# Performance work log

Hardware: AMD Instinct MI355X
Metric: run time of the kernel (lower is better)

Reference implementation:

```python
import jax, jax.numpy as jnp
import numpy as np

VOCAB = 10000
EMBED = 100
T = 80
UNITS = 512
B = 4096
RATE = 0.2  # Keras LSTMCell dropout on inputs, 4 gate masks, cached across timesteps


def setup_inputs() -> dict:
    key = jax.random.key(0)
    ks = jax.random.split(key, 10)
    s = 0.05
    return {
        "inputs": jax.random.randint(ks[0], (B, T), 0, VOCAB, dtype=jnp.int32),
        "embed": jax.random.normal(ks[1], (VOCAB, EMBED), dtype=jnp.float32) * s,
        "W0": jax.random.normal(ks[2], (EMBED, 4 * UNITS), dtype=jnp.float32) * s,
        "U0": jax.random.normal(ks[3], (UNITS, 4 * UNITS), dtype=jnp.float32) * s,
        "b0": jnp.zeros((4 * UNITS,), dtype=jnp.float32),
        "W1": jax.random.normal(ks[4], (UNITS, 4 * UNITS), dtype=jnp.float32) * s,
        "U1": jax.random.normal(ks[5], (UNITS, 4 * UNITS), dtype=jnp.float32) * s,
        "b1": jnp.zeros((4 * UNITS,), dtype=jnp.float32),
        "Wout": jax.random.normal(ks[6], (UNITS, 1), dtype=jnp.float32) * s,
        "bout": jnp.zeros((1,), dtype=jnp.float32),
    }


def _dropout_masks(key, shape):
    keep = 1.0 - RATE
    return jax.random.bernoulli(key, keep, shape).astype(jnp.float32) / keep


def _lstm_cell(h, c, xt, masks, W, U, b, in_dim):
    # masks: [4, B, in_dim] per-gate input dropout masks (fixed across time)
    # kernel layout: W.reshape(in_dim, 4, UNITS), gate order i, f, g(cand), o
    z = jnp.einsum('gbd,dgh->bgh', xt[None] * masks, W.reshape(in_dim, 4, UNITS))
    z = z + (h @ U + b).reshape(-1, 4, UNITS)
    i = jax.nn.sigmoid(z[:, 0])
    f = jax.nn.sigmoid(z[:, 1])
    g = jnp.tanh(z[:, 2])
    o = jax.nn.sigmoid(z[:, 3])
    c_new = f * c + i * g
    h_new = o * jnp.tanh(c_new)
    return h_new, c_new


def reference(inputs, embed, W0, U0, b0, W1, U1, b1, Wout, bout):
    x = embed[inputs]                      # [B, T, EMBED]
    mkey = jax.random.key(42)
    k0, k1 = jax.random.split(mkey)
    m0 = _dropout_masks(k0, (4, B, EMBED))
    m1 = _dropout_masks(k1, (4, B, UNITS))

    def step(carry, xt):
        h0, c0, h1, c1 = carry
        h0, c0 = _lstm_cell(h0, c0, xt, m0, W0, U0, b0, EMBED)
        h1, c1 = _lstm_cell(h1, c1, h0, m1, W1, U1, b1, UNITS)
        return (h0, c0, h1, c1), None

    init = tuple(jnp.zeros((B, UNITS), dtype=jnp.float32) for _ in range(4))
    (h0, c0, h1, c1), _ = jax.lax.scan(step, init, jnp.swapaxes(x, 0, 1))
    return jax.nn.sigmoid(h1 @ Wout + bout)   # [B, 1]
```

## Files before the change

### kernel.cpp

```cpp
#include <hip/hip_runtime.h>
#include <hip/hip_bf16.h>
#include <stdint.h>

#define BATCH 4096
#define TT    80
#define EMB   100
#define UNITS 512
#define K0P   128

typedef unsigned short ushort;
typedef unsigned char uchar;
typedef __bf16 bf16x8 __attribute__((ext_vector_type(8)));
typedef float f32x4 __attribute__((ext_vector_type(4)));
typedef uint32_t u32x4 __attribute__((ext_vector_type(4)));

__device__ __forceinline__ uint32_t rotl32(uint32_t x, uint32_t r) {
  return (x << r) | (x >> (32u - r));
}
__device__ __forceinline__ void tf_round4(uint32_t& x0, uint32_t& x1,
                                          int r0, int r1, int r2, int r3) {
  x0 += x1; x1 = rotl32(x1, r0); x1 ^= x0;
  x0 += x1; x1 = rotl32(x1, r1); x1 ^= x0;
  x0 += x1; x1 = rotl32(x1, r2); x1 ^= x0;
  x0 += x1; x1 = rotl32(x1, r3); x1 ^= x0;
}
__device__ __forceinline__ void tf2x32(uint32_t k0, uint32_t k1,
                                       uint32_t x0, uint32_t x1,
                                       uint32_t& y0, uint32_t& y1) {
  uint32_t k2 = k0 ^ k1 ^ 0x1BD11BDAu;
  x0 += k0; x1 += k1;
  tf_round4(x0, x1, 13, 15, 26, 6);  x0 += k1; x1 += k2 + 1u;
  tf_round4(x0, x1, 17, 29, 16, 24); x0 += k2; x1 += k0 + 2u;
  tf_round4(x0, x1, 13, 15, 26, 6);  x0 += k0; x1 += k1 + 3u;
  tf_round4(x0, x1, 17, 29, 16, 24); x0 += k1; x1 += k2 + 4u;
  tf_round4(x0, x1, 13, 15, 26, 6);  x0 += k2; x1 += k0 + 5u;
  y0 = x0; y1 = x1;
}
__device__ __forceinline__ int keepbit(uint32_t u) {
  float f = __uint_as_float((u >> 9) | 0x3F800000u) - 1.0f;
  return f < 0.8f ? 1 : 0;
}
__device__ __forceinline__ ushort f2bf(float f) {
  uint32_t u = __float_as_uint(f);
  uint32_t r = (u + 0x7FFFu + ((u >> 16) & 1u)) >> 16;
  return (ushort)r;
}
__device__ __forceinline__ float bf2f(ushort u) {
  return __uint_as_float(((uint32_t)u) << 16);
}

__global__ __launch_bounds__(256) void masksB(uchar* __restrict__ m0B,
                                              uchar* __restrict__ m1B) {
  uint32_t k0a, k0b, k1a, k1b;
  tf2x32(0u, 42u, 0u, 0u, k0a, k0b);
  tf2x32(0u, 42u, 0u, 1u, k1a, k1b);
  const int T0 = 4 * BATCH * K0P;
  const int T1 = 4 * BATCH * UNITS;
  for (int i = blockIdx.x * blockDim.x + threadIdx.x; i < T0 + T1;
       i += gridDim.x * blockDim.x) {
    if (i < T0) {
      const int g = i >> 19, b = (i >> 7) & 4095, k = i & 127;
      uchar v = 0;
      if (k < EMB) {
        uint32_t y0, y1;
        tf2x32(k0a, k0b, 0u, (uint32_t)(g * (BATCH * EMB) + b * EMB + k), y0, y1);
        v = keepbit(y0 ^ y1) ? 0xFFu : 0u;
      }
      m0B[i] = v;
    } else {
      const int j = i - T0;
      const int g = j >> 21, b = (j >> 9) & 4095, k = j & 511;
      uint32_t y0, y1;
      tf2x32(k1a, k1b, 0u, (uint32_t)(g * (BATCH * UNITS) + b * UNITS + k), y0, y1);
      m1B[j] = keepbit(y0 ^ y1) ? 0xFFu : 0u;
    }
  }
}

__global__ __launch_bounds__(256) void convT(const float* __restrict__ src,
                                             ushort* __restrict__ dst,
                                             int Ksrc, int Kpad, float scale) {
  __shared__ float t[32][33];
  const int n0 = blockIdx.x * 32, kk0 = blockIdx.y * 32;
  const int tx = threadIdx.x & 31, ty = threadIdx.x >> 5;
#pragma unroll
  for (int r = ty; r < 32; r += 8) {
    const int k = kk0 + r;
    t[r][tx] = (k < Ksrc) ? src[(size_t)k * 2048 + n0 + tx] : 0.f;
  }
  __syncthreads();
#pragma unroll
  for (int r = ty; r < 32; r += 8)
    dst[(size_t)(n0 + r) * Kpad + kk0 + tx] = f2bf(scale * t[tx][r]);
}

__global__ __launch_bounds__(256) void xprep3(const int* __restrict__ inputs,
                                              const float* __restrict__ embed,
                                              ushort* __restrict__ X0,
                                              ushort* __restrict__ X1,
                                              ushort* __restrict__ X2) {
  const int i = blockIdx.x * 256 + threadIdx.x;
  const int s = i >> 16, r = i & 65535;
  const int b = r >> 4, k = (r & 15) * 8;
  ushort* X = (s == 0) ? X0 : (s == 1) ? X1 : X2;
  const int idx = inputs[b * TT + s];
  ushort v[8];
#pragma unroll
  for (int j = 0; j < 8; j++) {
    const int kk = k + j;
    v[j] = (kk < EMB) ? f2bf(embed[(size_t)idx * EMB + kk]) : (ushort)0;
  }
  *(bf16x8*)(X + (size_t)b * K0P + k) = *(bf16x8*)v;
}

__device__ __forceinline__ void gload16(const void* g, void* l) {
  __builtin_amdgcn_global_load_lds(
      (const __attribute__((address_space(1))) unsigned int*)g,
      (__attribute__((address_space(3))) unsigned int*)l, 16, 0, 0);
}

template <bool MASKED>
__device__ __forceinline__ void gemm_seg(
    const ushort* __restrict__ A, int K, const ushort* __restrict__ Bw,
    const uchar* __restrict__ mB, int bm0, int bh0, int tid,
    ushort* As, ushort* Bs, f32x4 acc[4][8]) {
  const int w = tid >> 6, l = tid & 63;
  const int wr = w >> 1, wc = w & 1;
  const int fr = l & 15, kq = l >> 4;
  const int srow = l >> 2, schunk = (l & 3) * 8;

#pragma unroll 1
  for (int k0 = 0; k0 < K; k0 += 32) {
#pragma unroll
    for (int c2 = 0; c2 < 2; c2++) {
      const int rt = w + c2 * 4;
      gload16(A + (size_t)(bm0 + rt * 16 + srow) * K + k0 + schunk,
              As + rt * 512);
    }
#pragma unroll
    for (int c2 = 0; c2 < 4; c2++) {
      const int ct = w * 4 + c2;
      const int col = ct * 16 + srow;
      const int nrow = (col >> 6) * 512 + bh0 + (col & 63);
      gload16(Bw + (size_t)nrow * K + k0 + schunk, Bs + ct * 512);
    }
    uint2 md[4][4];
    if (MASKED) {
#pragma unroll
      for (int fi = 0; fi < 4; fi++) {
        const int row = bm0 + wr * 64 + fi * 16 + fr;
#pragma unroll
        for (int g = 0; g < 4; g++)
          md[fi][g] = *(const uint2*)(mB + (size_t)(g * BATCH + row) * K + k0 +
                                      kq * 8);
      }
    }
    __syncthreads();

    u32x4 af[4];
    bf16x8 bf[8];
#pragma unroll
    for (int fi = 0; fi < 4; fi++)
      af[fi] = *(const u32x4*)&As[(wr * 64 + fi * 16 + fr) * 32 + kq * 8];
#pragma unroll
    for (int g = 0; g < 4; g++)
#pragma unroll
      for (int hf = 0; hf < 2; hf++)
        bf[g * 2 + hf] =
            *(const bf16x8*)&Bs[((g * 4 + wc * 2 + hf) * 16 + fr) * 32 + kq * 8];

#pragma unroll
    for (int g = 0; g < 4; g++) {
#pragma unroll
      for (int fi = 0; fi < 4; fi++) {
        u32x4 ua = af[fi];
        if (MASKED) {
          const uint2 m = md[fi][g];
          ua.x &= __builtin_amdgcn_perm(m.x, m.x, 0x01010000u);
          ua.y &= __builtin_amdgcn_perm(m.x, m.x, 0x03030202u);
          ua.z &= __builtin_amdgcn_perm(m.y, m.y, 0x01010000u);
          ua.w &= __builtin_amdgcn_perm(m.y, m.y, 0x03030202u);
        }
        const bf16x8 a = __builtin_bit_cast(bf16x8, ua);
        acc[fi][g * 2 + 0] = __builtin_amdgcn_mfma_f32_16x16x32_bf16(
            a, bf[g * 2 + 0], acc[fi][g * 2 + 0], 0, 0, 0);
        acc[fi][g * 2 + 1] = __builtin_amdgcn_mfma_f32_16x16x32_bf16(
            a, bf[g * 2 + 1], acc[fi][g * 2 + 1], 0, 0, 0);
      }
    }
    __syncthreads();
  }
}

__global__ __launch_bounds__(256, 2) void fused_step(
    int nl1,
    const ushort* __restrict__ h0b_cur, const ushort* __restrict__ h1b_prev,
    ushort* __restrict__ h1b_out, float* __restrict__ c1f,
    const ushort* __restrict__ W1T, const ushort* __restrict__ U1T,
    const float* __restrict__ b1, int nl0, const ushort* __restrict__ Xcur,
    ushort* __restrict__ h0b_out, float* __restrict__ c0f,
    const ushort* __restrict__ W0T, const ushort* __restrict__ U0T,
    const float* __restrict__ b0, const uchar* __restrict__ mask1B,
    const uchar* __restrict__ mask0B, int tprep, const int* __restrict__ inputs,
    const float* __restrict__ embed, ushort* __restrict__ Xprep) {
  __shared__ __align__(16) ushort smem[12288];
  const int bid = blockIdx.x, tid = threadIdx.x;
  const bool isl1 = bid < nl1;
  const int lbid = isl1 ? bid : bid - nl1;
  const int cid = (lbid & 7) * 32 + (lbid >> 3);
  const int bm0 = (cid >> 3) * 128;
  const int bh0 = (cid & 7) * 64;
  const int w = tid >> 6, l = tid & 63;
  const int wr = w >> 1, wc = w & 1;
  const int fr = l & 15, kq = l >> 4;

  const ushort *Amask, *Aun, *BW, *BU;
  const float* bias;
  const uchar* mB;
  float* cblob;
  ushort* hout;
  int Km;
  if (isl1) {
    Amask = h0b_cur; Km = UNITS; Aun = h1b_prev; BW = W1T; BU = U1T;
    bias = b1; mB = mask1B; cblob = c1f; hout = h1b_out;
  } else {
    Amask = Xcur; Km = K0P; Aun = h0b_cur; BW = W0T; BU = U0T;
    bias = b0; mB = mask0B; cblob = c0f; hout = h0b_out;
  }

  f32x4 acc[4][8] = {};
  ushort* As = smem;
  ushort* Bs = smem + 4096;

  gemm_seg<true>(Amask, Km, BW, mB, bm0, bh0, tid, As, Bs, acc);
  gemm_seg<false>(Aun, UNITS, BU, nullptr, bm0, bh0, tid, As, Bs, acc);

  float* cb = cblob + (size_t)cid * 8192 + tid * 32;
  f32x4 cold[8];
#pragma unroll
  for (int q = 0; q < 8; q++) cold[q] = *(const f32x4*)(cb + q * 4);

  float bi[2], bfv[2], bg[2], bo[2];
#pragma unroll
  for (int hf = 0; hf < 2; hf++) {
    const int h = bh0 + wc * 32 + hf * 16 + fr;
    bi[hf] = bias[h];
    bfv[hf] = bias[512 + h];
    bg[hf] = bias[1024 + h];
    bo[hf] = bias[1536 + h];
  }

  f32x4 cnew[8];
#pragma unroll
  for (int fi = 0; fi < 4; fi++) {
#pragma unroll
    for (int hf = 0; hf < 2; hf++) {
#pragma unroll
      for (int jj = 0; jj < 4; jj++) {
        const float zi = acc[fi][0 + hf][jj] + bi[hf];
        const float zf = acc[fi][2 + hf][jj] + bfv[hf];
        const float zg = acc[fi][4 + hf][jj] + bg[hf];
        const float zo = acc[fi][6 + hf][jj] + bo[hf];
        const float iv = 1.f / (1.f + __expf(-zi));
        const float fv = 1.f / (1.f + __expf(-zf));
        const float gv = tanhf(zg);
        const float ov = 1.f / (1.f + __expf(-zo));
        const float cn = fv * cold[fi * 2 + hf][jj] + iv * gv;
        cnew[fi * 2 + hf][jj] = cn;
        const float hn = ov * tanhf(cn);
        const int rloc = wr * 64 + fi * 16 + kq * 4 + jj;
        const int hloc = wc * 32 + hf * 16 + fr;
        smem[rloc * 64 + hloc] = f2bf(hn);
      }
    }
  }
#pragma unroll
  for (int q = 0; q < 8; q++) *(f32x4*)(cb + q * 4) = cnew[q];
  __syncthreads();

#pragma unroll
  for (int c2 = 0; c2 < 4; c2++) {
    const int idx = c2 * 256 + tid;
    const int rloc = idx >> 3, hcol = (idx & 7) * 8;
    *(bf16x8*)(hout + (size_t)(bm0 + rloc) * UNITS + bh0 + hcol) =
        *(const bf16x8*)&smem[rloc * 64 + hcol];
  }

  if (!isl1 && tprep >= 0) {
    const int base = lbid * 2048 + tid * 8;
    const int b = base >> 7, k = base & 127;
    const int idx = inputs[b * TT + tprep];
    ushort v[8];
#pragma unroll
    for (int j = 0; j < 8; j++) {
      const int kk = k + j;
      v[j] = (kk < EMB) ? f2bf(embed[(size_t)idx * EMB + kk]) : (ushort)0;
    }
    *(bf16x8*)(Xprep + (size_t)b * K0P + k) = *(bf16x8*)v;
  }
}

__global__ __launch_bounds__(256) void out_kernel(const ushort* __restrict__ h1b,
                                                  const float* __restrict__ Wout,
                                                  const float* __restrict__ bout,
                                                  float* __restrict__ out) {
  const int wid = (blockIdx.x * blockDim.x + threadIdx.x) >> 6;
  const int lane = threadIdx.x & 63;
  if (wid >= BATCH) return;
  const ushort* hr = h1b + (size_t)wid * UNITS;
  float s = 0.f;
#pragma unroll
  for (int j = 0; j < UNITS; j += 64) s += bf2f(hr[j + lane]) * Wout[j + lane];
  for (int off = 32; off; off >>= 1) s += __shfl_down(s, off, 64);
  if (lane == 0) out[wid] = 1.f / (1.f + __expf(-(s + bout[0])));
}

extern "C" void kernel_launch(void* const* d_in, const int* in_sizes, int n_in,
                              void* d_out, int out_size, void* d_ws, size_t ws_size,
                              hipStream_t stream) {
  const int* inputs = (const int*)d_in[0];
  const float* embed = (const float*)d_in[1];
  const float* W0 = (const float*)d_in[2];
  const float* U0 = (const float*)d_in[3];
  const float* b0 = (const float*)d_in[4];
  const float* W1 = (const float*)d_in[5];
  const float* U1 = (const float*)d_in[6];
  const float* b1 = (const float*)d_in[7];
  const float* Wout = (const float*)d_in[8];
  const float* bout = (const float*)d_in[9];
  float* out = (float*)d_out;

  char* ws = (char*)d_ws;
  const size_t MB = 1 << 20;
  float* c0f    = (float*)(ws);
  float* c1f    = (float*)(ws + 8 * MB);
  ushort* h0b1  = (ushort*)(ws + 16 * MB);
  ushort* h1b1  = (ushort*)(ws + 20 * MB);
  ushort* h0b0  = (ushort*)(ws + 24 * MB);
  ushort* h1b0  = (ushort*)(ws + 28 * MB);
  ushort* X0    = (ushort*)(ws + 32 * MB);
  ushort* X1    = (ushort*)(ws + 33 * MB);
  ushort* X2    = (ushort*)(ws + 34 * MB);
  ushort* W0T   = (ushort*)(ws + 35 * MB);
  ushort* U0T   = (ushort*)(ws + 36 * MB);
  ushort* W1T   = (ushort*)(ws + 38 * MB);
  ushort* U1T   = (ushort*)(ws + 40 * MB);
  uchar* m0B    = (uchar*)(ws + 42 * MB);
  uchar* m1B    = (uchar*)(ws + 44 * MB);

  ushort* h0b[2] = {h0b0, h0b1};
  ushort* h1b[2] = {h1b0, h1b1};
  ushort* X[3] = {X0, X1, X2};

  hipMemsetAsync(ws, 0, 24 * MB, stream);

  masksB<<<8192, 256, 0, stream>>>(m0B, m1B);
  {
    dim3 g0(2048 / 32, K0P / 32);
    convT<<<g0, 256, 0, stream>>>(W0, W0T, EMB, K0P, 1.25f);
    dim3 g1(2048 / 32, UNITS / 32);
    convT<<<g1, 256, 0, stream>>>(U0, U0T, UNITS, UNITS, 1.0f);
    convT<<<g1, 256, 0, stream>>>(W1, W1T, UNITS, UNITS, 1.25f);
    convT<<<g1, 256, 0, stream>>>(U1, U1T, UNITS, UNITS, 1.0f);
  }
  xprep3<<<768, 256, 0, stream>>>(inputs, embed, X0, X1, X2);

  fused_step<<<256, 256, 0, stream>>>(
      0, h0b[1], h1b[1], h1b[0], c1f, W1T, U1T, b1,
      256, X[0], h0b[0], c0f, W0T, U0T, b0, m1B, m0B,
      -1, inputs, embed, X[0]);

  for (int k = 0; k < TT; k++) {
    const int p = k & 1;
    const int nl0 = (k < TT - 1) ? 256 : 0;
    const int tprep = (k + 3 < TT) ? (k + 3) : -1;
    fused_step<<<256 + nl0, 256, 0, stream>>>(
        256, h0b[p], h1b[p ^ 1], h1b[p], c1f, W1T, U1T, b1,
        nl0, X[(k + 1) % 3], h0b[p ^ 1], c0f, W0T, U0T, b0, m1B, m0B,
        tprep, inputs, embed, X[k % 3]);
  }

  out_kernel<<<BATCH * 64 / 256, 256, 0, stream>>>(h1b[1], Wout, bout, out);
}
```

Before: 6.276 ms.

## Replace per-timestep launches with a persistent kernel using a global atomic barrier

The 81 per-step fused_step launches become one persistent kernel of 512 blocks. Blocks loop over the phases and sync through a spin-wait atomic grid barrier. The cell state now stays in registers across steps instead of round-tripping through global memory, and embedding prefetch moves to a double buffer. The mask loads move inside the MFMA loop to cut register pressure. This removes launch overhead and c-state traffic, but relies on all 512 blocks being co-resident (2 per CU) and adds barrier latency.

```diff
diff --git a/kernel.cpp b/kernel.cpp
--- a/kernel.cpp
+++ b/kernel.cpp
@@ -7,6 +7,7 @@
 #define EMB   100
 #define UNITS 512
 #define K0P   128
+#define NBLK  512
 
 typedef unsigned short ushort;
 typedef unsigned char uchar;
@@ -94,21 +95,22 @@
     dst[(size_t)(n0 + r) * Kpad + kk0 + tx] = f2bf(scale * t[tx][r]);
 }
 
-__global__ __launch_bounds__(256) void xprep3(const int* __restrict__ inputs,
+__global__ __launch_bounds__(256) void xprep2(const int* __restrict__ inputs,
                                               const float* __restrict__ embed,
-                                              ushort* __restrict__ X0,
-                                              ushort* __restrict__ X1,
-                                              ushort* __restrict__ X2) {
+                                              ushort* __restrict__ XA,
+                                              ushort* __restrict__ XB) {
   const int i = blockIdx.x * 256 + threadIdx.x;
   const int s = i >> 16, r = i & 65535;
   const int b = r >> 4, k = (r & 15) * 8;
-  ushort* X = (s == 0) ? X0 : (s == 1) ? X1 : X2;
+  ushort* X = s ? XB : XA;
   const int idx = inputs[b * TT + s];
   ushort v[8];
 #pragma unroll
   for (int j = 0; j < 8; j++) {
     const int kk = k + j;
-    v[j] = (kk < EMB) ? f2bf(embed[(size_t)idx * EMB + kk]) : (ushort)0;
+    float f = 0.f;
+    if (kk < EMB) f = embed[(size_t)idx * EMB + kk];
+    v[j] = f2bf(f);
   }
   *(bf16x8*)(X + (size_t)b * K0P + k) = *(bf16x8*)v;
 }
@@ -144,38 +146,24 @@
       const int nrow = (col >> 6) * 512 + bh0 + (col & 63);
       gload16(Bw + (size_t)nrow * K + k0 + schunk, Bs + ct * 512);
     }
-    uint2 md[4][4];
-    if (MASKED) {
-#pragma unroll
-      for (int fi = 0; fi < 4; fi++) {
-        const int row = bm0 + wr * 64 + fi * 16 + fr;
-#pragma unroll
-        for (int g = 0; g < 4; g++)
-          md[fi][g] = *(const uint2*)(mB + (size_t)(g * BATCH + row) * K + k0 +
-                                      kq * 8);
-      }
-    }
     __syncthreads();
-
     u32x4 af[4];
-    bf16x8 bf[8];
 #pragma unroll
     for (int fi = 0; fi < 4; fi++)
       af[fi] = *(const u32x4*)&As[(wr * 64 + fi * 16 + fr) * 32 + kq * 8];
 #pragma unroll
-    for (int g = 0; g < 4; g++)
-#pragma unroll
-      for (int hf = 0; hf < 2; hf++)
-        bf[g * 2 + hf] =
-            *(const bf16x8*)&Bs[((g * 4 + wc * 2 + hf) * 16 + fr) * 32 + kq * 8];
-
-#pragma unroll
     for (int g = 0; g < 4; g++) {
+      const bf16x8 b0v =
+          *(const bf16x8*)&Bs[((g * 4 + wc * 2 + 0) * 16 + fr) * 32 + kq * 8];
+      const bf16x8 b1v =
+          *(const bf16x8*)&Bs[((g * 4 + wc * 2 + 1) * 16 + fr) * 32 + kq * 8];
 #pragma unroll
       for (int fi = 0; fi < 4; fi++) {
         u32x4 ua = af[fi];
         if (MASKED) {
-          const uint2 m = md[fi][g];
+          const int row = bm0 + wr * 64 + fi * 16 + fr;
+          const uint2 m =
+              *(const uint2*)(mB + (size_t)(g * BATCH + row) * K + k0 + kq * 8);
           ua.x &= __builtin_amdgcn_perm(m.x, m.x, 0x01010000u);
           ua.y &= __builtin_amdgcn_perm(m.x, m.x, 0x03030202u);
           ua.z &= __builtin_amdgcn_perm(m.y, m.y, 0x01010000u);
@@ -183,120 +171,142 @@
         }
         const bf16x8 a = __builtin_bit_cast(bf16x8, ua);
         acc[fi][g * 2 + 0] = __builtin_amdgcn_mfma_f32_16x16x32_bf16(
-            a, bf[g * 2 + 0], acc[fi][g * 2 + 0], 0, 0, 0);
+            a, b0v, acc[fi][g * 2 + 0], 0, 0, 0);
         acc[fi][g * 2 + 1] = __builtin_amdgcn_mfma_f32_16x16x32_bf16(
-            a, bf[g * 2 + 1], acc[fi][g * 2 + 1], 0, 0, 0);
+            a, b1v, acc[fi][g * 2 + 1], 0, 0, 0);
       }
     }
     __syncthreads();
   }
 }
 
-__global__ __launch_bounds__(256, 2) void fused_step(
-    int nl1,
-    const ushort* __restrict__ h0b_cur, const ushort* __restrict__ h1b_prev,
-    ushort* __restrict__ h1b_out, float* __restrict__ c1f,
-    const ushort* __restrict__ W1T, const ushort* __restrict__ U1T,
-    const float* __restrict__ b1, int nl0, const ushort* __restrict__ Xcur,
-    ushort* __restrict__ h0b_out, float* __restrict__ c0f,
+__device__ __forceinline__ void gbar(unsigned* cnt, unsigned target) {
+  __syncthreads();
+  if (threadIdx.x == 0) {
+    __builtin_amdgcn_fence(__ATOMIC_RELEASE, "agent");
+    __hip_atomic_fetch_add(cnt, 1u, __ATOMIC_RELAXED, __HIP_MEMORY_SCOPE_AGENT);
+    unsigned v;
+    int it = 0;
+    do {
+      __builtin_amdgcn_s_sleep(2);
+      v = __hip_atomic_load(cnt, __ATOMIC_RELAXED, __HIP_MEMORY_SCOPE_AGENT);
+    } while (v < target && ++it < 10000000);
+    __builtin_amdgcn_fence(__ATOMIC_ACQUIRE, "agent");
+  }
+  __syncthreads();
+}
+
+__global__ __launch_bounds__(256, 2) void lstm_persist(
     const ushort* __restrict__ W0T, const ushort* __restrict__ U0T,
-    const float* __restrict__ b0, const uchar* __restrict__ mask1B,
-    const uchar* __restrict__ mask0B, int tprep, const int* __restrict__ inputs,
-    const float* __restrict__ embed, ushort* __restrict__ Xprep) {
+    const float* __restrict__ b0, const ushort* __restrict__ W1T,
+    const ushort* __restrict__ U1T, const float* __restrict__ b1,
+    const uchar* __restrict__ m0B, const uchar* __restrict__ m1B,
+    ushort* __restrict__ h0A, ushort* __restrict__ h0B_,
+    ushort* __restrict__ h1A, ushort* __restrict__ h1B_,
+    ushort* __restrict__ XA, ushort* __restrict__ XB,
+    const int* __restrict__ inputs, const float* __restrict__ embed,
+    unsigned* __restrict__ barcnt) {
   __shared__ __align__(16) ushort smem[12288];
   const int bid = blockIdx.x, tid = threadIdx.x;
-  const bool isl1 = bid < nl1;
-  const int lbid = isl1 ? bid : bid - nl1;
-  const int cid = (lbid & 7) * 32 + (lbid >> 3);
-  const int bm0 = (cid >> 3) * 128;
-  const int bh0 = (cid & 7) * 64;
+  const int x = bid & 7, j = bid >> 3;
+  const bool isl1 = j & 1;
+  const int mblk = x * 4 + ((j >> 1) & 3);
+  const int nblk = j >> 3;
+  const int bm0 = mblk * 128, bh0 = nblk * 64;
   const int w = tid >> 6, l = tid & 63;
   const int wr = w >> 1, wc = w & 1;
   const int fr = l & 15, kq = l >> 4;
 
-  const ushort *Amask, *Aun, *BW, *BU;
-  const float* bias;
-  const uchar* mB;
-  float* cblob;
-  ushort* hout;
-  int Km;
-  if (isl1) {
-    Amask = h0b_cur; Km = UNITS; Aun = h1b_prev; BW = W1T; BU = U1T;
-    bias = b1; mB = mask1B; cblob = c1f; hout = h1b_out;
-  } else {
-    Amask = Xcur; Km = K0P; Aun = h0b_cur; BW = W0T; BU = U0T;
-    bias = b0; mB = mask0B; cblob = c0f; hout = h0b_out;
-  }
-
-  f32x4 acc[4][8] = {};
-  ushort* As = smem;
-  ushort* Bs = smem + 4096;
-
-  gemm_seg<true>(Amask, Km, BW, mB, bm0, bh0, tid, As, Bs, acc);
-  gemm_seg<false>(Aun, UNITS, BU, nullptr, bm0, bh0, tid, As, Bs, acc);
-
-  float* cb = cblob + (size_t)cid * 8192 + tid * 32;
-  f32x4 cold[8];
-#pragma unroll
-  for (int q = 0; q < 8; q++) cold[q] = *(const f32x4*)(cb + q * 4);
+  ushort* h0buf[2] = {h0A, h0B_};
+  ushort* h1buf[2] = {h1A, h1B_};
+  ushort* Xbuf[2] = {XA, XB};
+
+  f32x4 cfr[8];
+#pragma unroll
+  for (int q = 0; q < 8; q++) cfr[q] = f32x4{0.f, 0.f, 0.f, 0.f};
 
   float bi[2], bfv[2], bg[2], bo[2];
-#pragma unroll
-  for (int hf = 0; hf < 2; hf++) {
-    const int h = bh0 + wc * 32 + hf * 16 + fr;
-    bi[hf] = bias[h];
-    bfv[hf] = bias[512 + h];
-    bg[hf] = bias[1024 + h];
-    bo[hf] = bias[1536 + h];
-  }
-
-  f32x4 cnew[8];
-#pragma unroll
-  for (int fi = 0; fi < 4; fi++) {
+  {
+    const float* bias = isl1 ? b1 : b0;
 #pragma unroll
     for (int hf = 0; hf < 2; hf++) {
-#pragma unroll
-      for (int jj = 0; jj < 4; jj++) {
-        const float zi = acc[fi][0 + hf][jj] + bi[hf];
-        const float zf = acc[fi][2 + hf][jj] + bfv[hf];
-        const float zg = acc[fi][4 + hf][jj] + bg[hf];
-        const float zo = acc[fi][6 + hf][jj] + bo[hf];
-        const float iv = 1.f / (1.f + __expf(-zi));
-        const float fv = 1.f / (1.f + __expf(-zf));
-        const float gv = tanhf(zg);
-        const float ov = 1.f / (1.f + __expf(-zo));
-        const float cn = fv * cold[fi * 2 + hf][jj] + iv * gv;
-        cnew[fi * 2 + hf][jj] = cn;
-        const float hn = ov * tanhf(cn);
-        const int rloc = wr * 64 + fi * 16 + kq * 4 + jj;
-        const int hloc = wc * 32 + hf * 16 + fr;
-        smem[rloc * 64 + hloc] = f2bf(hn);
-      }
-    }
-  }
-#pragma unroll
-  for (int q = 0; q < 8; q++) *(f32x4*)(cb + q * 4) = cnew[q];
-  __syncthreads();
-
-#pragma unroll
-  for (int c2 = 0; c2 < 4; c2++) {
-    const int idx = c2 * 256 + tid;
-    const int rloc = idx >> 3, hcol = (idx & 7) * 8;
-    *(bf16x8*)(hout + (size_t)(bm0 + rloc) * UNITS + bh0 + hcol) =
-        *(const bf16x8*)&smem[rloc * 64 + hcol];
-  }
-
-  if (!isl1 && tprep >= 0) {
-    const int base = lbid * 2048 + tid * 8;
-    const int b = base >> 7, k = base & 127;
-    const int idx = inputs[b * TT + tprep];
-    ushort v[8];
-#pragma unroll
-    for (int j = 0; j < 8; j++) {
-      const int kk = k + j;
-      v[j] = (kk < EMB) ? f2bf(embed[(size_t)idx * EMB + kk]) : (ushort)0;
-    }
-    *(bf16x8*)(Xprep + (size_t)b * K0P + k) = *(bf16x8*)v;
+      const int h = bh0 + wc * 32 + hf * 16 + fr;
+      bi[hf] = bias[h];
+      bfv[hf] = bias[512 + h];
+      bg[hf] = bias[1024 + h];
+      bo[hf] = bias[1536 + h];
+    }
+  }
+
+#pragma unroll 1
+  for (int ph = 0; ph <= 80; ph++) {
+    const int p = ph & 1;
+    const bool active = isl1 ? (ph >= 1) : (ph <= 79);
+    if (active) {
+      f32x4 acc[4][8] = {};
+      if (isl1) {
+        gemm_seg<true>(h0buf[p ^ 1], UNITS, W1T, m1B, bm0, bh0, tid, smem,
+                       smem + 4096, acc);
+        gemm_seg<false>(h1buf[p ^ 1], UNITS, U1T, nullptr, bm0, bh0, tid, smem,
+                        smem + 4096, acc);
+      } else {
+        gemm_seg<true>(Xbuf[p], K0P, W0T, m0B, bm0, bh0, tid, smem,
+                       smem + 4096, acc);
+        gemm_seg<false>(h0buf[p ^ 1], UNITS, U0T, nullptr, bm0, bh0, tid, smem,
+                        smem + 4096, acc);
+      }
+      ushort* hout = isl1 ? h1buf[p] : h0buf[p];
+#pragma unroll
+      for (int fi = 0; fi < 4; fi++) {
+#pragma unroll
+        for (int hf = 0; hf < 2; hf++) {
+#pragma unroll
+          for (int jj = 0; jj < 4; jj++) {
+            const float zi = acc[fi][0 + hf][jj] + bi[hf];
+            const float zf = acc[fi][2 + hf][jj] + bfv[hf];
+            const float zg = acc[fi][4 + hf][jj] + bg[hf];
+            const float zo = acc[fi][6 + hf][jj] + bo[hf];
+            const float iv = 1.f / (1.f + __expf(-zi));
+            const float fv = 1.f / (1.f + __expf(-zf));
+            const float gv = tanhf(zg);
+            const float ov = 1.f / (1.f + __expf(-zo));
+            const float cn = fv * cfr[fi * 2 + hf][jj] + iv * gv;
+            cfr[fi * 2 + hf][jj] = cn;
+            const float hn = ov * tanhf(cn);
+            smem[(wr * 64 + fi * 16 + kq * 4 + jj) * 64 + wc * 32 + hf * 16 +
+                 fr] = f2bf(hn);
+          }
+        }
+      }
+      __syncthreads();
+#pragma unroll
+      for (int c2 = 0; c2 < 4; c2++) {
+        const int idx = c2 * 256 + tid;
+        const int rloc = idx >> 3, hcol = (idx & 7) * 8;
+        *(bf16x8*)(hout + (size_t)(bm0 + rloc) * UNITS + bh0 + hcol) =
+            *(const bf16x8*)&smem[rloc * 64 + hcol];
+      }
+      if (!isl1 && ph + 2 <= 79) {
+        const int r = tid >> 1, half = tid & 1;
+        const int row = bm0 + r;
+        const int idx = inputs[row * TT + ph + 2];
+        ushort* dst = Xbuf[p] + (size_t)row * K0P + half * 64;
+        const float* src = embed + (size_t)idx * EMB + half * 64;
+#pragma unroll
+        for (int kk = 0; kk < 64; kk += 8) {
+          ushort v[8];
+#pragma unroll
+          for (int q2 = 0; q2 < 8; q2++) {
+            const int col = half * 64 + kk + q2;
+            float f = 0.f;
+            if (col < EMB) f = src[kk + q2];
+            v[q2] = f2bf(f);
+          }
+          *(bf16x8*)(dst + kk) = *(bf16x8*)v;
+        }
+      }
+    }
+    if (ph < 80) gbar(barcnt, (unsigned)(ph + 1) * (unsigned)NBLK);
   }
 }
 
@@ -332,27 +342,22 @@
 
   char* ws = (char*)d_ws;
   const size_t MB = 1 << 20;
-  float* c0f    = (float*)(ws);
-  float* c1f    = (float*)(ws + 8 * MB);
-  ushort* h0b1  = (ushort*)(ws + 16 * MB);
-  ushort* h1b1  = (ushort*)(ws + 20 * MB);
-  ushort* h0b0  = (ushort*)(ws + 24 * MB);
-  ushort* h1b0  = (ushort*)(ws + 28 * MB);
-  ushort* X0    = (ushort*)(ws + 32 * MB);
-  ushort* X1    = (ushort*)(ws + 33 * MB);
-  ushort* X2    = (ushort*)(ws + 34 * MB);
-  ushort* W0T   = (ushort*)(ws + 35 * MB);
-  ushort* U0T   = (ushort*)(ws + 36 * MB);
-  ushort* W1T   = (ushort*)(ws + 38 * MB);
-  ushort* U1T   = (ushort*)(ws + 40 * MB);
-  uchar* m0B    = (uchar*)(ws + 42 * MB);
-  uchar* m1B    = (uchar*)(ws + 44 * MB);
-
-  ushort* h0b[2] = {h0b0, h0b1};
-  ushort* h1b[2] = {h1b0, h1b1};
-  ushort* X[3] = {X0, X1, X2};
-
-  hipMemsetAsync(ws, 0, 24 * MB, stream);
+  ushort* h0A  = (ushort*)(ws + 0 * MB);
+  ushort* h0B_ = (ushort*)(ws + 4 * MB);
+  ushort* h1A  = (ushort*)(ws + 8 * MB);
+  ushort* h1B_ = (ushort*)(ws + 12 * MB);
+  ushort* XA   = (ushort*)(ws + 16 * MB);
+  ushort* XB   = (ushort*)(ws + 17 * MB);
+  ushort* W0T  = (ushort*)(ws + 18 * MB);
+  ushort* U0T  = (ushort*)(ws + 19 * MB);
+  ushort* W1T  = (ushort*)(ws + 21 * MB);
+  ushort* U1T  = (ushort*)(ws + 23 * MB);
+  uchar* m0B   = (uchar*)(ws + 25 * MB);
+  uchar* m1B   = (uchar*)(ws + 27 * MB);
+  unsigned* barcnt = (unsigned*)(ws + 35 * MB);
+
+  hipMemsetAsync(ws + 4 * MB, 0, 8 * MB, stream);
+  hipMemsetAsync(barcnt, 0, 4096, stream);
 
   masksB<<<8192, 256, 0, stream>>>(m0B, m1B);
   {
@@ -363,22 +368,11 @@
     convT<<<g1, 256, 0, stream>>>(W1, W1T, UNITS, UNITS, 1.25f);
     convT<<<g1, 256, 0, stream>>>(U1, U1T, UNITS, UNITS, 1.0f);
   }
-  xprep3<<<768, 256, 0, stream>>>(inputs, embed, X0, X1, X2);
-
-  fused_step<<<256, 256, 0, stream>>>(
-      0, h0b[1], h1b[1], h1b[0], c1f, W1T, U1T, b1,
-      256, X[0], h0b[0], c0f, W0T, U0T, b0, m1B, m0B,
-      -1, inputs, embed, X[0]);
-
-  for (int k = 0; k < TT; k++) {
-    const int p = k & 1;
-    const int nl0 = (k < TT - 1) ? 256 : 0;
-    const int tprep = (k + 3 < TT) ? (k + 3) : -1;
-    fused_step<<<256 + nl0, 256, 0, stream>>>(
-        256, h0b[p], h1b[p ^ 1], h1b[p], c1f, W1T, U1T, b1,
-        nl0, X[(k + 1) % 3], h0b[p ^ 1], c0f, W0T, U0T, b0, m1B, m0B,
-        tprep, inputs, embed, X[k % 3]);
-  }
-
-  out_kernel<<<BATCH * 64 / 256, 256, 0, stream>>>(h1b[1], Wout, bout, out);
-}
+  xprep2<<<512, 256, 0, stream>>>(inputs, embed, XA, XB);
+
+  lstm_persist<<<NBLK, 256, 0, stream>>>(W0T, U0T, b0, W1T, U1T, b1, m0B, m1B,
+                                         h0A, h0B_, h1A, h1B_, XA, XB, inputs,
+                                         embed, barcnt);
+
+  out_kernel<<<BATCH * 64 / 256, 256, 0, stream>>>(h1A, Wout, bout, out);
+}
```

Result: slower. 11.43 ms (+82.1%).

## Pre-tile operands into MFMA fragment layout and double-buffer LDS in fused LSTM step

Applied to the files above, without the earlier changes.

Weights, embeddings and hidden states are stored in a 16x32 tile-major layout, so each wave's global-to-LDS load reads one contiguous 1 KB chunk instead of strided rows. The K loop is double-buffered, prefetching the next tile while the current one is multiplied. The per-block output tile shrinks from 64 to 32 hidden units, doubling the block count and halving the accumulators to raise occupancy. The exact tanhf is replaced by an exp-based fast tanh, and the next-step embedding prep is moved to a subset of blocks. The cost is extra retiling kernels at setup and possible small numeric differences from the fast tanh.

```diff
diff --git a/kernel.cpp b/kernel.cpp
--- a/kernel.cpp
+++ b/kernel.cpp
@@ -13,6 +13,10 @@
 typedef __bf16 bf16x8 __attribute__((ext_vector_type(8)));
 typedef float f32x4 __attribute__((ext_vector_type(4)));
 typedef uint32_t u32x4 __attribute__((ext_vector_type(4)));
+
+#define TOFF(r, k, KT)                                                  \
+  ((((size_t)((r) >> 4) * (KT) + ((k) >> 5)) << 9) +                    \
+   ((((k) >> 3) & 3) << 7) + (((r) & 15) << 3) + ((k) & 7))
 
 __device__ __forceinline__ uint32_t rotl32(uint32_t x, uint32_t r) {
   return (x << r) | (x >> (32u - r));
@@ -47,6 +51,12 @@
 }
 __device__ __forceinline__ float bf2f(ushort u) {
   return __uint_as_float(((uint32_t)u) << 16);
+}
+__device__ __forceinline__ float fast_tanh(float x) {
+  const float ax = fabsf(x);
+  const float t = __expf(-2.f * ax);
+  const float r = (1.f - t) / (1.f + t);
+  return copysignf(r, x);
 }
 
 __global__ __launch_bounds__(256) void masksB(uchar* __restrict__ m0B,
@@ -94,23 +104,31 @@
     dst[(size_t)(n0 + r) * Kpad + kk0 + tx] = f2bf(scale * t[tx][r]);
 }
 
-__global__ __launch_bounds__(256) void xprep3(const int* __restrict__ inputs,
+__global__ __launch_bounds__(256) void retileB(const ushort* __restrict__ lin,
+                                               ushort* __restrict__ til, int K) {
+  const int id = blockIdx.x * 256 + threadIdx.x;
+  const int r = id / (K >> 3);
+  const int kc = id % (K >> 3);
+  bf16x8 v = *(const bf16x8*)(lin + (size_t)r * K + kc * 8);
+  *(bf16x8*)(til + TOFF(r, kc * 8, K >> 5)) = v;
+}
+
+__global__ __launch_bounds__(256) void xprep2(const int* __restrict__ inputs,
                                               const float* __restrict__ embed,
-                                              ushort* __restrict__ X0,
-                                              ushort* __restrict__ X1,
-                                              ushort* __restrict__ X2) {
+                                              ushort* __restrict__ XA,
+                                              ushort* __restrict__ XB) {
   const int i = blockIdx.x * 256 + threadIdx.x;
-  const int s = i >> 16, r = i & 65535;
-  const int b = r >> 4, k = (r & 15) * 8;
-  ushort* X = (s == 0) ? X0 : (s == 1) ? X1 : X2;
+  const int s = i >> 16, rem = i & 65535;
+  const int b = rem >> 4, kc = rem & 15;
+  ushort* X = s ? XB : XA;
   const int idx = inputs[b * TT + s];
   ushort v[8];
 #pragma unroll
   for (int j = 0; j < 8; j++) {
-    const int kk = k + j;
+    const int kk = kc * 8 + j;
     v[j] = (kk < EMB) ? f2bf(embed[(size_t)idx * EMB + kk]) : (ushort)0;
   }
-  *(bf16x8*)(X + (size_t)b * K0P + k) = *(bf16x8*)v;
+  *(bf16x8*)(X + TOFF(b, kc * 8, 4)) = *(bf16x8*)v;
 }
 
 __device__ __forceinline__ void gload16(const void* g, void* l) {
@@ -119,184 +137,188 @@
       (__attribute__((address_space(3))) unsigned int*)l, 16, 0, 0);
 }
 
-template <bool MASKED>
-__device__ __forceinline__ void gemm_seg(
-    const ushort* __restrict__ A, int K, const ushort* __restrict__ Bw,
-    const uchar* __restrict__ mB, int bm0, int bh0, int tid,
-    ushort* As, ushort* Bs, f32x4 acc[4][8]) {
+__global__ __launch_bounds__(256) void fused_step(
+    int nl1, int nl0,
+    const ushort* __restrict__ h0m, const ushort* __restrict__ h1p,
+    ushort* __restrict__ h1o, float* __restrict__ c1f,
+    const ushort* __restrict__ W1T, const ushort* __restrict__ U1T,
+    const float* __restrict__ b1, const uchar* __restrict__ m1B,
+    const ushort* __restrict__ Xc, const ushort* __restrict__ h0p,
+    ushort* __restrict__ h0o, float* __restrict__ c0f,
+    const ushort* __restrict__ W0T, const ushort* __restrict__ U0T,
+    const float* __restrict__ b0, const uchar* __restrict__ m0B,
+    int tprep, const int* __restrict__ inputs, const float* __restrict__ embed,
+    ushort* __restrict__ Xprep) {
+  __shared__ __align__(16) ushort smem[16384];
+  const int bid = blockIdx.x, tid = threadIdx.x;
+  const bool isl1 = bid < nl1;
+  const int lbid = isl1 ? bid : bid - nl1;
+  const int cid = (lbid & 7) * 64 + (lbid >> 3);
+  const int mblk = cid >> 4, nblk = cid & 15;
+  const int bm0 = mblk * 128, bh0 = nblk * 32;
+  const int rtb = bm0 >> 4;
+  const int nb2 = nblk * 2;
   const int w = tid >> 6, l = tid & 63;
   const int wr = w >> 1, wc = w & 1;
   const int fr = l & 15, kq = l >> 4;
-  const int srow = l >> 2, schunk = (l & 3) * 8;
+
+  const ushort *A1, *B1, *A2, *B2;
+  const uchar* mB;
+  const float* bias;
+  float* cb;
+  ushort* hout;
+  int KTA1, S1, K1;
+  if (isl1) {
+    A1 = h0m; B1 = W1T; A2 = h1p; B2 = U1T; mB = m1B; bias = b1;
+    cb = c1f; hout = h1o; KTA1 = 16; S1 = 16; K1 = 512;
+  } else {
+    A1 = Xc; B1 = W0T; A2 = h0p; B2 = U0T; mB = m0B; bias = b0;
+    cb = c0f; hout = h0o; KTA1 = 4; S1 = 4; K1 = 128;
+  }
+  const int S = S1 + 16;
+
+  f32x4 acc[4][4] = {};
+  f32x4 cold[4];
+
+#pragma unroll
+  for (int c2 = 0; c2 < 2; c2++) {
+    const int rt = w + c2 * 4;
+    gload16(A1 + ((size_t)(rtb + rt) * KTA1) * 512 + l * 8, smem + rt * 512);
+    const int nt = (rt >> 1) * 32 + nb2 + (rt & 1);
+    gload16(B1 + ((size_t)nt * KTA1) * 512 + l * 8, smem + 4096 + rt * 512);
+  }
+  __syncthreads();
 
 #pragma unroll 1
-  for (int k0 = 0; k0 < K; k0 += 32) {
-#pragma unroll
-    for (int c2 = 0; c2 < 2; c2++) {
-      const int rt = w + c2 * 4;
-      gload16(A + (size_t)(bm0 + rt * 16 + srow) * K + k0 + schunk,
-              As + rt * 512);
-    }
-#pragma unroll
-    for (int c2 = 0; c2 < 4; c2++) {
-      const int ct = w * 4 + c2;
-      const int col = ct * 16 + srow;
-      const int nrow = (col >> 6) * 512 + bh0 + (col & 63);
-      gload16(Bw + (size_t)nrow * K + k0 + schunk, Bs + ct * 512);
-    }
+  for (int s = 0; s < S; s++) {
+    ushort* cur = smem + (s & 1) * 8192;
+    ushort* nxt = smem + ((s & 1) ^ 1) * 8192;
+
     uint2 md[4][4];
-    if (MASKED) {
+    const bool masked = s < S1;
+    if (masked) {
+      const int kb = s * 32 + kq * 8;
 #pragma unroll
       for (int fi = 0; fi < 4; fi++) {
         const int row = bm0 + wr * 64 + fi * 16 + fr;
+        const uchar* mrow = mB + (size_t)row * K1 + kb;
 #pragma unroll
         for (int g = 0; g < 4; g++)
-          md[fi][g] = *(const uint2*)(mB + (size_t)(g * BATCH + row) * K + k0 +
-                                      kq * 8);
+          md[fi][g] = *(const uint2*)(mrow + (size_t)g * (BATCH * K1));
       }
     }
-    __syncthreads();
+
+    if (s + 1 < S) {
+      const bool m2 = (s + 1 < S1);
+      const ushort* A = m2 ? A1 : A2;
+      const ushort* B = m2 ? B1 : B2;
+      const int KT = m2 ? KTA1 : 16;
+      const int kt = m2 ? (s + 1) : (s + 1 - S1);
+#pragma unroll
+      for (int c2 = 0; c2 < 2; c2++) {
+        const int rt = w + c2 * 4;
+        gload16(A + ((size_t)(rtb + rt) * KT + kt) * 512 + l * 8,
+                nxt + rt * 512);
+        const int nt = (rt >> 1) * 32 + nb2 + (rt & 1);
+        gload16(B + ((size_t)nt * KT + kt) * 512 + l * 8,
+                nxt + 4096 + rt * 512);
+      }
+    }
+    if (s == S - 3) {
+      const float* cbase = cb + ((size_t)cid * 256 + tid) * 16;
+#pragma unroll
+      for (int q = 0; q < 4; q++) cold[q] = *(const f32x4*)(cbase + q * 4);
+    }
 
     u32x4 af[4];
-    bf16x8 bf[8];
+    bf16x8 bfr[4];
 #pragma unroll
     for (int fi = 0; fi < 4; fi++)
-      af[fi] = *(const u32x4*)&As[(wr * 64 + fi * 16 + fr) * 32 + kq * 8];
+      af[fi] = *(const u32x4*)&cur[(wr * 4 + fi) * 512 + l * 8];
 #pragma unroll
     for (int g = 0; g < 4; g++)
-#pragma unroll
-      for (int hf = 0; hf < 2; hf++)
-        bf[g * 2 + hf] =
-            *(const bf16x8*)&Bs[((g * 4 + wc * 2 + hf) * 16 + fr) * 32 + kq * 8];
-
-#pragma unroll
-    for (int g = 0; g < 4; g++) {
+      bfr[g] = *(const bf16x8*)&cur[4096 + (g * 2 + wc) * 512 + l * 8];
+
+    if (masked) {
 #pragma unroll
       for (int fi = 0; fi < 4; fi++) {
-        u32x4 ua = af[fi];
-        if (MASKED) {
+#pragma unroll
+        for (int g = 0; g < 4; g++) {
           const uint2 m = md[fi][g];
+          u32x4 ua = af[fi];
           ua.x &= __builtin_amdgcn_perm(m.x, m.x, 0x01010000u);
           ua.y &= __builtin_amdgcn_perm(m.x, m.x, 0x03030202u);
           ua.z &= __builtin_amdgcn_perm(m.y, m.y, 0x01010000u);
           ua.w &= __builtin_amdgcn_perm(m.y, m.y, 0x03030202u);
+          acc[fi][g] = __builtin_amdgcn_mfma_f32_16x16x32_bf16(
+              __builtin_bit_cast(bf16x8, ua), bfr[g], acc[fi][g], 0, 0, 0);
         }
-        const bf16x8 a = __builtin_bit_cast(bf16x8, ua);
-        acc[fi][g * 2 + 0] = __builtin_amdgcn_mfma_f32_16x16x32_bf16(
-            a, bf[g * 2 + 0], acc[fi][g * 2 + 0], 0, 0, 0);
-        acc[fi][g * 2 + 1] = __builtin_amdgcn_mfma_f32_16x16x32_bf16(
-            a, bf[g * 2 + 1], acc[fi][g * 2 + 1], 0, 0, 0);
       }
+    } else {
+#pragma unroll
+      for (int fi = 0; fi < 4; fi++)
+#pragma unroll
+        for (int g = 0; g < 4; g++)
+          acc[fi][g] = __builtin_amdgcn_mfma_f32_16x16x32_bf16(
+              __builtin_bit_cast(bf16x8, af[fi]), bfr[g], acc[fi][g], 0, 0, 0);
     }
     __syncthreads();
   }
-}
-
-__global__ __launch_bounds__(256, 2) void fused_step(
-    int nl1,
-    const ushort* __restrict__ h0b_cur, const ushort* __restrict__ h1b_prev,
-    ushort* __restrict__ h1b_out, float* __restrict__ c1f,
-    const ushort* __restrict__ W1T, const ushort* __restrict__ U1T,
-    const float* __restrict__ b1, int nl0, const ushort* __restrict__ Xcur,
-    ushort* __restrict__ h0b_out, float* __restrict__ c0f,
-    const ushort* __restrict__ W0T, const ushort* __restrict__ U0T,
-    const float* __restrict__ b0, const uchar* __restrict__ mask1B,
-    const uchar* __restrict__ mask0B, int tprep, const int* __restrict__ inputs,
-    const float* __restrict__ embed, ushort* __restrict__ Xprep) {
-  __shared__ __align__(16) ushort smem[12288];
-  const int bid = blockIdx.x, tid = threadIdx.x;
-  const bool isl1 = bid < nl1;
-  const int lbid = isl1 ? bid : bid - nl1;
-  const int cid = (lbid & 7) * 32 + (lbid >> 3);
-  const int bm0 = (cid >> 3) * 128;
-  const int bh0 = (cid & 7) * 64;
-  const int w = tid >> 6, l = tid & 63;
-  const int wr = w >> 1, wc = w & 1;
-  const int fr = l & 15, kq = l >> 4;
-
-  const ushort *Amask, *Aun, *BW, *BU;
-  const float* bias;
-  const uchar* mB;
-  float* cblob;
-  ushort* hout;
-  int Km;
-  if (isl1) {
-    Amask = h0b_cur; Km = UNITS; Aun = h1b_prev; BW = W1T; BU = U1T;
-    bias = b1; mB = mask1B; cblob = c1f; hout = h1b_out;
-  } else {
-    Amask = Xcur; Km = K0P; Aun = h0b_cur; BW = W0T; BU = U0T;
-    bias = b0; mB = mask0B; cblob = c0f; hout = h0b_out;
-  }
-
-  f32x4 acc[4][8] = {};
-  ushort* As = smem;
-  ushort* Bs = smem + 4096;
-
-  gemm_seg<true>(Amask, Km, BW, mB, bm0, bh0, tid, As, Bs, acc);
-  gemm_seg<false>(Aun, UNITS, BU, nullptr, bm0, bh0, tid, As, Bs, acc);
-
-  float* cb = cblob + (size_t)cid * 8192 + tid * 32;
-  f32x4 cold[8];
-#pragma unroll
-  for (int q = 0; q < 8; q++) cold[q] = *(const f32x4*)(cb + q * 4);
-
-  float bi[2], bfv[2], bg[2], bo[2];
-#pragma unroll
-  for (int hf = 0; hf < 2; hf++) {
-    const int h = bh0 + wc * 32 + hf * 16 + fr;
-    bi[hf] = bias[h];
-    bfv[hf] = bias[512 + h];
-    bg[hf] = bias[1024 + h];
-    bo[hf] = bias[1536 + h];
-  }
-
-  f32x4 cnew[8];
+
+  float bi, bfv, bg, bo;
+  {
+    const int h = bh0 + wc * 16 + fr;
+    bi = bias[h]; bfv = bias[512 + h]; bg = bias[1024 + h]; bo = bias[1536 + h];
+  }
+  f32x4 cnew[4];
 #pragma unroll
   for (int fi = 0; fi < 4; fi++) {
 #pragma unroll
-    for (int hf = 0; hf < 2; hf++) {
-#pragma unroll
-      for (int jj = 0; jj < 4; jj++) {
-        const float zi = acc[fi][0 + hf][jj] + bi[hf];
-        const float zf = acc[fi][2 + hf][jj] + bfv[hf];
-        const float zg = acc[fi][4 + hf][jj] + bg[hf];
-        const float zo = acc[fi][6 + hf][jj] + bo[hf];
-        const float iv = 1.f / (1.f + __expf(-zi));
-        const float fv = 1.f / (1.f + __expf(-zf));
-        const float gv = tanhf(zg);
-        const float ov = 1.f / (1.f + __expf(-zo));
-        const float cn = fv * cold[fi * 2 + hf][jj] + iv * gv;
-        cnew[fi * 2 + hf][jj] = cn;
-        const float hn = ov * tanhf(cn);
-        const int rloc = wr * 64 + fi * 16 + kq * 4 + jj;
-        const int hloc = wc * 32 + hf * 16 + fr;
-        smem[rloc * 64 + hloc] = f2bf(hn);
+    for (int jj = 0; jj < 4; jj++) {
+      const float zi = acc[fi][0][jj] + bi;
+      const float zf = acc[fi][1][jj] + bfv;
+      const float zg = acc[fi][2][jj] + bg;
+      const float zo = acc[fi][3][jj] + bo;
+      const float iv = 1.f / (1.f + __expf(-zi));
+      const float fv = 1.f / (1.f + __expf(-zf));
+      const float gv = fast_tanh(zg);
+      const float ov = 1.f / (1.f + __expf(-zo));
+      const float cn = fv * cold[fi][jj] + iv * gv;
+      cnew[fi][jj] = cn;
+      const float hn = ov * fast_tanh(cn);
+      smem[(wr * 64 + fi * 16 + kq * 4 + jj) * 32 + wc * 16 + fr] = f2bf(hn);
+    }
+  }
+  {
+    float* cbase = cb + ((size_t)cid * 256 + tid) * 16;
+#pragma unroll
+    for (int q = 0; q < 4; q++) *(f32x4*)(cbase + q * 4) = cnew[q];
+  }
+  __syncthreads();
+
+#pragma unroll
+  for (int c2 = 0; c2 < 2; c2++) {
+    const int u = tid * 2 + c2;
+    const int r = u >> 2, kc = u & 3;
+    *(bf16x8*)(hout + TOFF(bm0 + r, bh0 + kc * 8, 16)) =
+        *(const bf16x8*)&smem[r * 32 + kc * 8];
+  }
+
+  if (!isl1 && nblk == 0 && tprep >= 0) {
+#pragma unroll 1
+    for (int u2 = 0; u2 < 8; u2++) {
+      const int id = tid * 8 + u2;
+      const int rl = id >> 4, kc = id & 15;
+      const int row = bm0 + rl;
+      const int idx = inputs[row * TT + tprep];
+      ushort v[8];
+#pragma unroll
+      for (int j = 0; j < 8; j++) {
+        const int kk = kc * 8 + j;
+        v[j] = (kk < EMB) ? f2bf(embed[(size_t)idx * EMB + kk]) : (ushort)0;
       }
-    }
-  }
-#pragma unroll
-  for (int q = 0; q < 8; q++) *(f32x4*)(cb + q * 4) = cnew[q];
-  __syncthreads();
-
-#pragma unroll
-  for (int c2 = 0; c2 < 4; c2++) {
-    const int idx = c2 * 256 + tid;
-    const int rloc = idx >> 3, hcol = (idx & 7) * 8;
-    *(bf16x8*)(hout + (size_t)(bm0 + rloc) * UNITS + bh0 + hcol) =
-        *(const bf16x8*)&smem[rloc * 64 + hcol];
-  }
-
-  if (!isl1 && tprep >= 0) {
-    const int base = lbid * 2048 + tid * 8;
-    const int b = base >> 7, k = base & 127;
-    const int idx = inputs[b * TT + tprep];
-    ushort v[8];
-#pragma unroll
-    for (int j = 0; j < 8; j++) {
-      const int kk = k + j;
-      v[j] = (kk < EMB) ? f2bf(embed[(size_t)idx * EMB + kk]) : (ushort)0;
-    }
-    *(bf16x8*)(Xprep + (size_t)b * K0P + k) = *(bf16x8*)v;
+      *(bf16x8*)(Xprep + TOFF(row, kc * 8, 4)) = *(bf16x8*)v;
+    }
   }
 }
 
@@ -304,13 +326,16 @@
                                                   const float* __restrict__ Wout,
                                                   const float* __restrict__ bout,
                                                   float* __restrict__ out) {
-  const int wid = (blockIdx.x * blockDim.x + threadIdx.x) >> 6;
+  const int wid = (blockIdx.x * 256 + threadIdx.x) >> 6;
   const int lane = threadIdx.x & 63;
   if (wid >= BATCH) return;
-  const ushort* hr = h1b + (size_t)wid * UNITS;
+  const int rt = wid >> 4, rl = wid & 15;
+  const int kt = lane >> 2, ch = lane & 3;
+  const ushort* p = h1b + (((size_t)(rt * 16 + kt)) << 9) + (ch << 7) + (rl << 3);
+  const int kbase = kt * 32 + ch * 8;
   float s = 0.f;
 #pragma unroll
-  for (int j = 0; j < UNITS; j += 64) s += bf2f(hr[j + lane]) * Wout[j + lane];
+  for (int e = 0; e < 8; e++) s += bf2f(p[e]) * Wout[kbase + e];
   for (int off = 32; off; off >>= 1) s += __shfl_down(s, off, 64);
   if (lane == 0) out[wid] = 1.f / (1.f + __expf(-(s + bout[0])));
 }
@@ -332,21 +357,22 @@
 
   char* ws = (char*)d_ws;
   const size_t MB = 1 << 20;
-  float* c0f    = (float*)(ws);
-  float* c1f    = (float*)(ws + 8 * MB);
-  ushort* h0b1  = (ushort*)(ws + 16 * MB);
-  ushort* h1b1  = (ushort*)(ws + 20 * MB);
-  ushort* h0b0  = (ushort*)(ws + 24 * MB);
-  ushort* h1b0  = (ushort*)(ws + 28 * MB);
-  ushort* X0    = (ushort*)(ws + 32 * MB);
-  ushort* X1    = (ushort*)(ws + 33 * MB);
-  ushort* X2    = (ushort*)(ws + 34 * MB);
-  ushort* W0T   = (ushort*)(ws + 35 * MB);
-  ushort* U0T   = (ushort*)(ws + 36 * MB);
-  ushort* W1T   = (ushort*)(ws + 38 * MB);
-  ushort* U1T   = (ushort*)(ws + 40 * MB);
-  uchar* m0B    = (uchar*)(ws + 42 * MB);
-  uchar* m1B    = (uchar*)(ws + 44 * MB);
+  float* c0f   = (float*)(ws);
+  float* c1f   = (float*)(ws + 8 * MB);
+  ushort* h0b1 = (ushort*)(ws + 16 * MB);
+  ushort* h1b1 = (ushort*)(ws + 20 * MB);
+  ushort* h0b0 = (ushort*)(ws + 24 * MB);
+  ushort* h1b0 = (ushort*)(ws + 28 * MB);
+  ushort* X0   = (ushort*)(ws + 32 * MB);
+  ushort* X1   = (ushort*)(ws + 33 * MB);
+  ushort* X2   = (ushort*)(ws + 34 * MB);
+  ushort* W0T  = (ushort*)(ws + 35 * MB);
+  ushort* U0T  = (ushort*)(ws + 36 * MB);
+  ushort* W1T  = (ushort*)(ws + 38 * MB);
+  ushort* U1T  = (ushort*)(ws + 40 * MB);
+  ushort* tmp  = (ushort*)(ws + 42 * MB);
+  uchar* m0B   = (uchar*)(ws + 44 * MB);
+  uchar* m1B   = (uchar*)(ws + 46 * MB);
 
   ushort* h0b[2] = {h0b0, h0b1};
   ushort* h1b[2] = {h1b0, h1b1};
@@ -356,28 +382,32 @@
 
   masksB<<<8192, 256, 0, stream>>>(m0B, m1B);
   {
-    dim3 g0(2048 / 32, K0P / 32);
-    convT<<<g0, 256, 0, stream>>>(W0, W0T, EMB, K0P, 1.25f);
-    dim3 g1(2048 / 32, UNITS / 32);
-    convT<<<g1, 256, 0, stream>>>(U0, U0T, UNITS, UNITS, 1.0f);
-    convT<<<g1, 256, 0, stream>>>(W1, W1T, UNITS, UNITS, 1.25f);
-    convT<<<g1, 256, 0, stream>>>(U1, U1T, UNITS, UNITS, 1.0f);
-  }
-  xprep3<<<768, 256, 0, stream>>>(inputs, embed, X0, X1, X2);
-
-  fused_step<<<256, 256, 0, stream>>>(
-      0, h0b[1], h1b[1], h1b[0], c1f, W1T, U1T, b1,
-      256, X[0], h0b[0], c0f, W0T, U0T, b0, m1B, m0B,
-      -1, inputs, embed, X[0]);
+    dim3 g0(2048 / 32, K0P / 32), g1(2048 / 32, UNITS / 32);
+    convT<<<g0, 256, 0, stream>>>(W0, tmp, EMB, K0P, 1.25f);
+    retileB<<<(2048 * K0P / 8) / 256, 256, 0, stream>>>(tmp, W0T, K0P);
+    convT<<<g1, 256, 0, stream>>>(U0, tmp, UNITS, UNITS, 1.0f);
+    retileB<<<(2048 * UNITS / 8) / 256, 256, 0, stream>>>(tmp, U0T, UNITS);
+    convT<<<g1, 256, 0, stream>>>(W1, tmp, UNITS, UNITS, 1.25f);
+    retileB<<<(2048 * UNITS / 8) / 256, 256, 0, stream>>>(tmp, W1T, UNITS);
+    convT<<<g1, 256, 0, stream>>>(U1, tmp, UNITS, UNITS, 1.0f);
+    retileB<<<(2048 * UNITS / 8) / 256, 256, 0, stream>>>(tmp, U1T, UNITS);
+  }
+  xprep2<<<512, 256, 0, stream>>>(inputs, embed, X0, X1);
+
+  fused_step<<<512, 256, 0, stream>>>(
+      0, 512, h0b[1], h1b[1], h1b[0], c1f, W1T, U1T, b1, m1B,
+      X[0], h0b[1], h0b[0], c0f, W0T, U0T, b0, m0B,
+      2, inputs, embed, X[2]);
 
   for (int k = 0; k < TT; k++) {
     const int p = k & 1;
-    const int nl0 = (k < TT - 1) ? 256 : 0;
-    const int tprep = (k + 3 < TT) ? (k + 3) : -1;
-    fused_step<<<256 + nl0, 256, 0, stream>>>(
-        256, h0b[p], h1b[p ^ 1], h1b[p], c1f, W1T, U1T, b1,
-        nl0, X[(k + 1) % 3], h0b[p ^ 1], c0f, W0T, U0T, b0, m1B, m0B,
-        tprep, inputs, embed, X[k % 3]);
+    const int nl0 = (k < TT - 1) ? 512 : 0;
+    const int tp = (k + 3 < TT) ? (k + 3) : -1;
+    fused_step<<<512 + nl0, 256, 0, stream>>>(
+        512, nl0,
+        h0b[p], h1b[p ^ 1], h1b[p], c1f, W1T, U1T, b1, m1B,
+        X[(k + 1) % 3], h0b[p], h0b[p ^ 1], c0f, W0T, U0T, b0, m0B,
+        tp, inputs, embed, X[k % 3]);
   }
 
   out_kernel<<<BATCH * 64 / 256, 256, 0, stream>>>(h1b[1], Wout, bout, out);
```

Result: slower. 13.26 ms (+111.3%).
